# Optimization experiments

Hardware: AMD Instinct MI355X
Metric: run time of the kernel (lower is better)

Reference implementation:

```python
import jax, jax.numpy as jnp
import numpy as np

# Structure matrix S (n_hos*n_types=6, n_structures=8) and internal int_S (unused in forward)
S_MAT = np.array([[1,0,1,0,0,1,0,1],[0,1,0,1,1,0,0,0],[1,1,0,0,0,0,1,0],[0,0,1,1,0,1,0,0],[0,1,1,0,1,0,0,1],[1,0,0,0,1,0,1,0]], dtype=np.float32)
CONTROL_STRENGTH = 10.0  # self.control_strength
PDHG_ITERS = 150         # fixed-iteration batched primal-dual LP solver
BATCH = 32768
N_STRUCT = 8
N_COMBO = 6


def setup_inputs() -> dict:
    key = jax.random.key(0)
    ks = jax.random.split(key, 9)
    X = jax.random.uniform(ks[0], (BATCH, 2, 3), jnp.float32)  # nonnegative bids
    def lin(k, fan_in, fan_out):
        return jax.random.normal(k, (fan_in, fan_out), jnp.float32) * (1.0 / np.sqrt(fan_in))
    W1 = lin(ks[1], 6, 20);  b1 = jnp.zeros((20,), jnp.float32)
    W2 = lin(ks[2], 20, 20); b2 = jnp.zeros((20,), jnp.float32)
    W3 = lin(ks[3], 20, 20); b3 = jnp.zeros((20,), jnp.float32)
    W4 = lin(ks[4], 20, 8);  b4 = jnp.zeros((8,), jnp.float32)
    S = jnp.asarray(S_MAT)
    return {"X": X, "W1": W1, "b1": b1, "W2": W2, "b2": b2, "W3": W3, "b3": b3,
            "W4": W4, "b4": b4, "S": S, "batch_size": BATCH}


def _mlp(Z, W1, b1, W2, b2, W3, b3, W4, b4):
    h = jnp.tanh(Z @ W1 + b1)
    h = jnp.tanh(h @ W2 + b2)
    h = jnp.tanh(h @ W3 + b3)
    return h @ W4 + b4  # [B, 8]


def _batched_lp(S, z, bvec):
    """Solve, per batch row: max 1'x - c*||x - z||_2  s.t. x>=0, S x <= b.
    Equivalent polytope A x <= b' with A=[S; -I], b'=[b; 0]; solved with PDHG.
    z, bvec: [B, 8], [B, 6]."""
    B = z.shape[0]
    A = jnp.concatenate([S, -jnp.eye(N_STRUCT, dtype=S.dtype)], axis=0)  # [14, 8]
    bfull = jnp.concatenate([bvec, jnp.zeros((B, N_STRUCT), bvec.dtype)], axis=1)  # [B, 14]
    L = jnp.linalg.norm(A)  # Frobenius norm upper-bounds spectral norm
    tau = 1.0 / L
    sigma = 1.0 / L

    def prox_g(v):
        # prox of g(x) = -1'x + c||x - z||_2 (w = ones): shift by tau*w then shrink toward z
        u = v + tau
        d = u - z
        n = jnp.linalg.norm(d, axis=-1, keepdims=True)
        scale = jnp.maximum(0.0, 1.0 - tau * CONTROL_STRENGTH / jnp.maximum(n, 1e-12))
        return z + scale * d

    x0 = jnp.maximum(z, 0.0)
    y0 = jnp.zeros((B, N_COMBO + N_STRUCT), z.dtype)

    def step(carry, _):
        x, xbar, y = carry
        y = jnp.maximum(0.0, y + sigma * (xbar @ A.T - bfull))  # dual ascent + proj >= 0
        x_new = prox_g(x - tau * (y @ A))                        # primal prox step
        return (x_new, 2.0 * x_new - x, y), None

    (x, _, _), _ = jax.lax.scan(step, (x0, x0, y0), None, length=PDHG_ITERS)
    return x


def reference(X, W1, b1, W2, b2, W3, b3, W4, b4, S, batch_size):
    B = X.shape[0]
    Z = X.reshape(B, N_COMBO)              # view(-1, n_hos*n_types)
    z = _mlp(Z, W1, b1, W2, b2, W3, b3, W4, b4)  # neural_net_forward -> [B, 8]
    x1 = _batched_lp(S, z, Z)              # linear_program_forward (W = ones)
    return x1
```

## Files before the change

### kernel.cpp

```cpp
#include <hip/hip_runtime.h>
#include <math.h>


#define N_ITERS 150

__device__ __forceinline__ float fast_tanh(float a) {
    float e = __expf(2.0f * a);
    return 1.0f - 2.0f * __builtin_amdgcn_rcpf(e + 1.0f);
}

__global__ void __launch_bounds__(64)
__attribute__((amdgpu_waves_per_eu(1, 1)))
matchnet_kernel(
    const float* __restrict__ X,
    const float* __restrict__ W1, const float* __restrict__ b1,
    const float* __restrict__ W2, const float* __restrict__ b2,
    const float* __restrict__ W3, const float* __restrict__ b3,
    const float* __restrict__ W4, const float* __restrict__ b4,
    float* __restrict__ out, int B)
{
    __shared__ float sW1[120], sW2[400], sW3[400], sW4[160];
    __shared__ float sb1[20], sb2[20], sb3[20], sb4[8];
    for (int i = threadIdx.x; i < 120; i += blockDim.x) sW1[i] = W1[i];
    for (int i = threadIdx.x; i < 400; i += blockDim.x) sW2[i] = W2[i];
    for (int i = threadIdx.x; i < 400; i += blockDim.x) sW3[i] = W3[i];
    for (int i = threadIdx.x; i < 160; i += blockDim.x) sW4[i] = W4[i];
    if (threadIdx.x < 20) {
        sb1[threadIdx.x] = b1[threadIdx.x];
        sb2[threadIdx.x] = b2[threadIdx.x];
        sb3[threadIdx.x] = b3[threadIdx.x];
    }
    if (threadIdx.x < 8) sb4[threadIdx.x] = b4[threadIdx.x];
    __syncthreads();

    int row = blockIdx.x * blockDim.x + threadIdx.x;
    if (row >= B) return;

    float bb0 = X[row * 6 + 0], bb1 = X[row * 6 + 1], bb2 = X[row * 6 + 2];
    float bb3 = X[row * 6 + 3], bb4 = X[row * 6 + 4], bb5 = X[row * 6 + 5];

    float h1[20], h2[20];
    #pragma unroll
    for (int j = 0; j < 20; j++) {
        float acc = sb1[j];
        acc = fmaf(bb0, sW1[0 * 20 + j], acc);
        acc = fmaf(bb1, sW1[1 * 20 + j], acc);
        acc = fmaf(bb2, sW1[2 * 20 + j], acc);
        acc = fmaf(bb3, sW1[3 * 20 + j], acc);
        acc = fmaf(bb4, sW1[4 * 20 + j], acc);
        acc = fmaf(bb5, sW1[5 * 20 + j], acc);
        h1[j] = fast_tanh(acc);
    }
    #pragma unroll
    for (int j = 0; j < 20; j++) {
        float acc = sb2[j];
        #pragma unroll
        for (int i = 0; i < 20; i++) acc = fmaf(h1[i], sW2[i * 20 + j], acc);
        h2[j] = fast_tanh(acc);
    }
    #pragma unroll
    for (int j = 0; j < 20; j++) {
        float acc = sb3[j];
        #pragma unroll
        for (int i = 0; i < 20; i++) acc = fmaf(h2[i], sW3[i * 20 + j], acc);
        h1[j] = fast_tanh(acc);
    }
    float z0, z1, z2, z3, z4, z5, z6, z7;
    {
        float zt[8];
        #pragma unroll
        for (int k = 0; k < 8; k++) {
            float acc = sb4[k];
            #pragma unroll
            for (int i = 0; i < 20; i++) acc = fmaf(h1[i], sW4[i * 8 + k], acc);
            zt[k] = acc;
        }
        z0 = zt[0]; z1 = zt[1]; z2 = zt[2]; z3 = zt[3];
        z4 = zt[4]; z5 = zt[5]; z6 = zt[6]; z7 = zt[7];
    }

    const float tau  = 0.18898223650461363f;
    const float c    = 0.03571428571428571f;
    const float tauC = 1.8898223650461363f;

    float cb0 = c * bb0, cb1 = c * bb1, cb2 = c * bb2;
    float cb3 = c * bb3, cb4 = c * bb4, cb5 = c * bb5;

    float t0 = tau - z0, t1 = tau - z1, t2 = tau - z2, t3 = tau - z3;
    float t4 = tau - z4, t5 = tau - z5, t6 = tau - z6, t7 = tau - z7;
    float TI0 = t0, TI1 = t1, TI2 = t2, TI3 = t3;
    float TI4 = t4, TI5 = t5, TI6 = t6, TI7 = t7;

    float x0 = fmaxf(z0, 0.0f), x1 = fmaxf(z1, 0.0f), x2 = fmaxf(z2, 0.0f), x3 = fmaxf(z3, 0.0f);
    float x4 = fmaxf(z4, 0.0f), x5 = fmaxf(z5, 0.0f), x6 = fmaxf(z6, 0.0f), x7 = fmaxf(z7, 0.0f);
    float xb0 = x0, xb1 = x1, xb2 = x2, xb3 = x3, xb4 = x4, xb5 = x5, xb6 = x6, xb7 = x7;
    float Y0 = 0.f, Y1 = 0.f, Y2 = 0.f, Y3 = 0.f, Y4 = 0.f, Y5 = 0.f;

    #pragma unroll 1
    for (int it = 0; it < N_ITERS; it++) {
        float t07 = xb0 + xb7, t25 = xb2 + xb5, t12 = xb1 + xb2;
        float t47 = xb4 + xb7, t34 = xb3 + xb4, t06 = xb0 + xb6;
        float s0 = t07 + t25, s1 = t34 + xb1, s2 = t06 + xb1;
        float s3 = t25 + xb3, s4 = t12 + t47, s5 = t06 + xb4;

        Y0 = fmaxf(0.f, fmaf(c, s0, Y0) - cb0);
        Y1 = fmaxf(0.f, fmaf(c, s1, Y1) - cb1);
        Y2 = fmaxf(0.f, fmaf(c, s2, Y2) - cb2);
        Y3 = fmaxf(0.f, fmaf(c, s3, Y3) - cb3);
        Y4 = fmaxf(0.f, fmaf(c, s4, Y4) - cb4);
        Y5 = fmaxf(0.f, fmaf(c, s5, Y5) - cb5);

        TI0 = fmaxf(t0, fmaf(-c, xb0, TI0));
        TI1 = fmaxf(t1, fmaf(-c, xb1, TI1));
        TI2 = fmaxf(t2, fmaf(-c, xb2, TI2));
        TI3 = fmaxf(t3, fmaf(-c, xb3, TI3));
        TI4 = fmaxf(t4, fmaf(-c, xb4, TI4));
        TI5 = fmaxf(t5, fmaf(-c, xb5, TI5));
        TI6 = fmaxf(t6, fmaf(-c, xb6, TI6));
        TI7 = fmaxf(t7, fmaf(-c, xb7, TI7));

        float r03 = Y0 + Y3, r25 = Y2 + Y5, r14 = Y1 + Y4;
        float c0 = r25 + Y0, c1 = r14 + Y2, c2 = r03 + Y4;
        float c3 = Y1 + Y3,  c4 = r14 + Y5, c7 = Y0 + Y4;

        float dA0 = x0 + TI0, dA1 = x1 + TI1, dA2 = x2 + TI2, dA3 = x3 + TI3;
        float dA4 = x4 + TI4, dA5 = x5 + TI5, dA6 = x6 + TI6, dA7 = x7 + TI7;
        float d0 = dA0 - c0, d1 = dA1 - c1, d2 = dA2 - c2, d3 = dA3 - c3;
        float d4 = dA4 - c4, d5 = dA5 - r03, d6 = dA6 - r25, d7 = dA7 - c7;

        float nsq = d0 * d0;
        nsq = fmaf(d1, d1, nsq);
        nsq = fmaf(d2, d2, nsq);
        nsq = fmaf(d3, d3, nsq);
        nsq = fmaf(d4, d4, nsq);
        nsq = fmaf(d5, d5, nsq);
        nsq = fmaf(d6, d6, nsq);
        nsq = fmaf(d7, d7, nsq);

        float rs = __builtin_amdgcn_rsqf(nsq);
        float scale = fmaxf(0.0f, fmaf(-tauC, rs, 1.0f));

        float xn0 = fmaf(scale, d0, z0), xn1 = fmaf(scale, d1, z1);
        float xn2 = fmaf(scale, d2, z2), xn3 = fmaf(scale, d3, z3);
        float xn4 = fmaf(scale, d4, z4), xn5 = fmaf(scale, d5, z5);
        float xn6 = fmaf(scale, d6, z6), xn7 = fmaf(scale, d7, z7);
        xb0 = fmaf(2.0f, xn0, -x0); x0 = xn0;
        xb1 = fmaf(2.0f, xn1, -x1); x1 = xn1;
        xb2 = fmaf(2.0f, xn2, -x2); x2 = xn2;
        xb3 = fmaf(2.0f, xn3, -x3); x3 = xn3;
        xb4 = fmaf(2.0f, xn4, -x4); x4 = xn4;
        xb5 = fmaf(2.0f, xn5, -x5); x5 = xn5;
        xb6 = fmaf(2.0f, xn6, -x6); x6 = xn6;
        xb7 = fmaf(2.0f, xn7, -x7); x7 = xn7;
    }

    float4* out4 = (float4*)out;
    out4[row * 2 + 0] = make_float4(x0, x1, x2, x3);
    out4[row * 2 + 1] = make_float4(x4, x5, x6, x7);
}

extern "C" void kernel_launch(void* const* d_in, const int* in_sizes, int n_in,
                              void* d_out, int out_size, void* d_ws, size_t ws_size,
                              hipStream_t stream) {
    const float* X  = (const float*)d_in[0];
    const float* W1 = (const float*)d_in[1];
    const float* b1 = (const float*)d_in[2];
    const float* W2 = (const float*)d_in[3];
    const float* b2 = (const float*)d_in[4];
    const float* W3 = (const float*)d_in[5];
    const float* b3 = (const float*)d_in[6];
    const float* W4 = (const float*)d_in[7];
    const float* b4 = (const float*)d_in[8];
    float* out = (float*)d_out;

    int B = in_sizes[0] / 6;
    const int block = 64;
    int grid = (B + block - 1) / block;
    hipLaunchKernelGGL(matchnet_kernel, dim3(grid), dim3(block), 0, stream,
                       X, W1, b1, W2, b2, W3, b3, W4, b4, out, B);
}
```

Baseline: 111.5 us.

## Split each batch row across two lanes with DPP exchange in PDHG loop

After: 104.6 us. 6.2% less time.

```diff
diff --git a/kernel.cpp b/kernel.cpp
--- a/kernel.cpp
+++ b/kernel.cpp
@@ -7,6 +7,13 @@
 __device__ __forceinline__ float fast_tanh(float a) {
     float e = __expf(2.0f * a);
     return 1.0f - 2.0f * __builtin_amdgcn_rcpf(e + 1.0f);
+}
+
+__device__ __forceinline__ float dpp_swap(float v) {
+    union { float f; int i; } u;
+    u.f = v;
+    u.i = __builtin_amdgcn_update_dpp(0, u.i, 0xB1, 0xF, 0xF, true);
+    return u.f;
 }
 
 __global__ void __launch_bounds__(64)
@@ -33,8 +40,10 @@
     if (threadIdx.x < 8) sb4[threadIdx.x] = b4[threadIdx.x];
     __syncthreads();
 
-    int row = blockIdx.x * blockDim.x + threadIdx.x;
+    int gidx = blockIdx.x * blockDim.x + threadIdx.x;
+    int row = gidx >> 1;
     if (row >= B) return;
+    const bool isOdd = (gidx & 1) != 0;
 
     float bb0 = X[row * 6 + 0], bb1 = X[row * 6 + 1], bb2 = X[row * 6 + 2];
     float bb3 = X[row * 6 + 3], bb4 = X[row * 6 + 4], bb5 = X[row * 6 + 5];
@@ -65,98 +74,106 @@
         for (int i = 0; i < 20; i++) acc = fmaf(h2[i], sW3[i * 20 + j], acc);
         h1[j] = fast_tanh(acc);
     }
-    float z0, z1, z2, z3, z4, z5, z6, z7;
-    {
-        float zt[8];
+    float z[8];
+    #pragma unroll
+    for (int k = 0; k < 8; k++) {
+        float acc = sb4[k];
         #pragma unroll
-        for (int k = 0; k < 8; k++) {
-            float acc = sb4[k];
-            #pragma unroll
-            for (int i = 0; i < 20; i++) acc = fmaf(h1[i], sW4[i * 8 + k], acc);
-            zt[k] = acc;
-        }
-        z0 = zt[0]; z1 = zt[1]; z2 = zt[2]; z3 = zt[3];
-        z4 = zt[4]; z5 = zt[5]; z6 = zt[6]; z7 = zt[7];
+        for (int i = 0; i < 20; i++) acc = fmaf(h1[i], sW4[i * 8 + k], acc);
+        z[k] = acc;
     }
 
     const float tau  = 0.18898223650461363f;
     const float c    = 0.03571428571428571f;
     const float tauC = 1.8898223650461363f;
 
+    float oz0 = isOdd ? z[4] : z[0];
+    float oz1 = isOdd ? z[5] : z[1];
+    float oz2 = isOdd ? z[6] : z[2];
+    float oz3 = isOdd ? z[7] : z[3];
+
+    float ot0 = tau - oz0, ot1 = tau - oz1, ot2 = tau - oz2, ot3 = tau - oz3;
+    float oTI0 = ot0, oTI1 = ot1, oTI2 = ot2, oTI3 = ot3;
+
+    float ox0 = fmaxf(oz0, 0.f), ox1 = fmaxf(oz1, 0.f);
+    float ox2 = fmaxf(oz2, 0.f), ox3 = fmaxf(oz3, 0.f);
+    float oxb0 = ox0, oxb1 = ox1, oxb2 = ox2, oxb3 = ox3;
+
     float cb0 = c * bb0, cb1 = c * bb1, cb2 = c * bb2;
     float cb3 = c * bb3, cb4 = c * bb4, cb5 = c * bb5;
-
-    float t0 = tau - z0, t1 = tau - z1, t2 = tau - z2, t3 = tau - z3;
-    float t4 = tau - z4, t5 = tau - z5, t6 = tau - z6, t7 = tau - z7;
-    float TI0 = t0, TI1 = t1, TI2 = t2, TI3 = t3;
-    float TI4 = t4, TI5 = t5, TI6 = t6, TI7 = t7;
-
-    float x0 = fmaxf(z0, 0.0f), x1 = fmaxf(z1, 0.0f), x2 = fmaxf(z2, 0.0f), x3 = fmaxf(z3, 0.0f);
-    float x4 = fmaxf(z4, 0.0f), x5 = fmaxf(z5, 0.0f), x6 = fmaxf(z6, 0.0f), x7 = fmaxf(z7, 0.0f);
-    float xb0 = x0, xb1 = x1, xb2 = x2, xb3 = x3, xb4 = x4, xb5 = x5, xb6 = x6, xb7 = x7;
-    float Y0 = 0.f, Y1 = 0.f, Y2 = 0.f, Y3 = 0.f, Y4 = 0.f, Y5 = 0.f;
+    float cbq0 = isOdd ? cb4 : cb0;
+    float cbq1 = isOdd ? cb3 : cb2;
+    float cbq2 = isOdd ? cb5 : cb1;
+    float Yq0 = 0.f, Yq1 = 0.f, Yq2 = 0.f;
 
     #pragma unroll 1
     for (int it = 0; it < N_ITERS; it++) {
-        float t07 = xb0 + xb7, t25 = xb2 + xb5, t12 = xb1 + xb2;
-        float t47 = xb4 + xb7, t34 = xb3 + xb4, t06 = xb0 + xb6;
-        float s0 = t07 + t25, s1 = t34 + xb1, s2 = t06 + xb1;
-        float s3 = t25 + xb3, s4 = t12 + t47, s5 = t06 + xb4;
+        float rxb0 = dpp_swap(oxb0), rxb1 = dpp_swap(oxb1);
+        float rxb2 = dpp_swap(oxb2), rxb3 = dpp_swap(oxb3);
 
-        Y0 = fmaxf(0.f, fmaf(c, s0, Y0) - cb0);
-        Y1 = fmaxf(0.f, fmaf(c, s1, Y1) - cb1);
-        Y2 = fmaxf(0.f, fmaf(c, s2, Y2) - cb2);
-        Y3 = fmaxf(0.f, fmaf(c, s3, Y3) - cb3);
-        Y4 = fmaxf(0.f, fmaf(c, s4, Y4) - cb4);
-        Y5 = fmaxf(0.f, fmaf(c, s5, Y5) - cb5);
+        float op_a = oxb0 + rxb1;
+        float op_b = oxb2 + rxb3;
+        float op_c = oxb3 + rxb2;
+        float op_d = isOdd ? op_c : op_b;
+        float sq0  = op_a + op_d;
+        float op_e = oxb1 + rxb2;
+        float op_f = isOdd ? rxb3 : oxb0;
+        float sq1  = op_e + op_f;
+        float op_g = oxb1 + oxb3;
+        float op_h = oxb0 + oxb2;
+        float op_i = isOdd ? op_h : op_g;
+        float sq2  = op_i + rxb0;
 
-        TI0 = fmaxf(t0, fmaf(-c, xb0, TI0));
-        TI1 = fmaxf(t1, fmaf(-c, xb1, TI1));
-        TI2 = fmaxf(t2, fmaf(-c, xb2, TI2));
-        TI3 = fmaxf(t3, fmaf(-c, xb3, TI3));
-        TI4 = fmaxf(t4, fmaf(-c, xb4, TI4));
-        TI5 = fmaxf(t5, fmaf(-c, xb5, TI5));
-        TI6 = fmaxf(t6, fmaf(-c, xb6, TI6));
-        TI7 = fmaxf(t7, fmaf(-c, xb7, TI7));
+        Yq0 = fmaxf(0.f, fmaf(c, sq0, Yq0) - cbq0);
+        Yq1 = fmaxf(0.f, fmaf(c, sq1, Yq1) - cbq1);
+        Yq2 = fmaxf(0.f, fmaf(c, sq2, Yq2) - cbq2);
 
-        float r03 = Y0 + Y3, r25 = Y2 + Y5, r14 = Y1 + Y4;
-        float c0 = r25 + Y0, c1 = r14 + Y2, c2 = r03 + Y4;
-        float c3 = Y1 + Y3,  c4 = r14 + Y5, c7 = Y0 + Y4;
+        float rY0 = dpp_swap(Yq0), rY1 = dpp_swap(Yq1), rY2 = dpp_swap(Yq2);
 
-        float dA0 = x0 + TI0, dA1 = x1 + TI1, dA2 = x2 + TI2, dA3 = x3 + TI3;
-        float dA4 = x4 + TI4, dA5 = x5 + TI5, dA6 = x6 + TI6, dA7 = x7 + TI7;
-        float d0 = dA0 - c0, d1 = dA1 - c1, d2 = dA2 - c2, d3 = dA3 - c3;
-        float d4 = dA4 - c4, d5 = dA5 - r03, d6 = dA6 - r25, d7 = dA7 - c7;
+        float op_j = Yq0 + rY2;
+        float op_k = isOdd ? Yq2 : Yq1;
+        float colq0 = op_j + op_k;
+        float op_l = Yq1 + rY0;
+        float op_p = isOdd ? 0.f : Yq2;
+        float colq1 = op_l + op_p;
+        float op_m = Yq0 + rY0;
+        float op_n = rY1 + Yq2;
+        float op_o = op_m + rY1;
+        float colq2 = isOdd ? op_n : op_o;
+        float colq3 = isOdd ? op_m : op_n;
 
-        float nsq = d0 * d0;
-        nsq = fmaf(d1, d1, nsq);
-        nsq = fmaf(d2, d2, nsq);
-        nsq = fmaf(d3, d3, nsq);
-        nsq = fmaf(d4, d4, nsq);
-        nsq = fmaf(d5, d5, nsq);
-        nsq = fmaf(d6, d6, nsq);
-        nsq = fmaf(d7, d7, nsq);
+        oTI0 = fmaxf(ot0, fmaf(-c, oxb0, oTI0));
+        oTI1 = fmaxf(ot1, fmaf(-c, oxb1, oTI1));
+        oTI2 = fmaxf(ot2, fmaf(-c, oxb2, oTI2));
+        oTI3 = fmaxf(ot3, fmaf(-c, oxb3, oTI3));
+
+        float od0 = (ox0 + oTI0) - colq0;
+        float od1 = (ox1 + oTI1) - colq1;
+        float od2 = (ox2 + oTI2) - colq2;
+        float od3 = (ox3 + oTI3) - colq3;
+
+        float nl = od0 * od0;
+        nl = fmaf(od1, od1, nl);
+        nl = fmaf(od2, od2, nl);
+        nl = fmaf(od3, od3, nl);
+        float rn = dpp_swap(nl);
+        float nsq = nl + rn;
 
         float rs = __builtin_amdgcn_rsqf(nsq);
-        float scale = fmaxf(0.0f, fmaf(-tauC, rs, 1.0f));
+        float scale = fmaxf(0.f, fmaf(-tauC, rs, 1.f));
 
-        float xn0 = fmaf(scale, d0, z0), xn1 = fmaf(scale, d1, z1);
-        float xn2 = fmaf(scale, d2, z2), xn3 = fmaf(scale, d3, z3);
-        float xn4 = fmaf(scale, d4, z4), xn5 = fmaf(scale, d5, z5);
-        float xn6 = fmaf(scale, d6, z6), xn7 = fmaf(scale, d7, z7);
-        xb0 = fmaf(2.0f, xn0, -x0); x0 = xn0;
-        xb1 = fmaf(2.0f, xn1, -x1); x1 = xn1;
-        xb2 = fmaf(2.0f, xn2, -x2); x2 = xn2;
-        xb3 = fmaf(2.0f, xn3, -x3); x3 = xn3;
-        xb4 = fmaf(2.0f, xn4, -x4); x4 = xn4;
-        xb5 = fmaf(2.0f, xn5, -x5); x5 = xn5;
-        xb6 = fmaf(2.0f, xn6, -x6); x6 = xn6;
-        xb7 = fmaf(2.0f, xn7, -x7); x7 = xn7;
+        float xn0 = fmaf(scale, od0, oz0);
+        float xn1 = fmaf(scale, od1, oz1);
+        float xn2 = fmaf(scale, od2, oz2);
+        float xn3 = fmaf(scale, od3, oz3);
+        oxb0 = fmaf(2.f, xn0, -ox0); ox0 = xn0;
+        oxb1 = fmaf(2.f, xn1, -ox1); ox1 = xn1;
+        oxb2 = fmaf(2.f, xn2, -ox2); ox2 = xn2;
+        oxb3 = fmaf(2.f, xn3, -ox3); ox3 = xn3;
     }
 
     float4* out4 = (float4*)out;
-    out4[row * 2 + 0] = make_float4(x0, x1, x2, x3);
-    out4[row * 2 + 1] = make_float4(x4, x5, x6, x7);
+    out4[gidx] = make_float4(ox0, ox1, ox2, ox3);
 }
 
 extern "C" void kernel_launch(void* const* d_in, const int* in_sizes, int n_in,
@@ -175,7 +192,8 @@
 
     int B = in_sizes[0] / 6;
     const int block = 64;
-    int grid = (B + block - 1) / block;
+    long long threads = (long long)B * 2;
+    int grid = (int)((threads + block - 1) / block);
     hipLaunchKernelGGL(matchnet_kernel, dim3(grid), dim3(block), 0, stream,
                        X, W1, b1, W2, b2, W3, b3, W4, b4, out, B);
 }
```
